# Kernel tuning notes

Measured on AMD Instinct MI355X. Metric: run time of the kernel, lower is better.

## Reference

```python
import jax, jax.numpy as jnp
import numpy as np
from jax import lax

ALPHA = 100.0      # SuperSpike surrogate slope (LIFParameters alpha)
DT = 1e-3          # norse default dt
TAU_SYN_INV = 200.0
TAU_MEM_INV = 100.0
V_TH = 1.0

@jax.custom_vjp
def superspike(x):
    return (x > 0).astype(x.dtype)

def _ss_fwd(x):
    return (x > 0).astype(x.dtype), x

def _ss_bwd(x, g):
    return (g / (ALPHA * jnp.abs(x) + 1.0) ** 2,)

superspike.defvjp(_ss_fwd, _ss_bwd)

def lif_step(inp, v, i):
    # norse lif_step: decay v/i, spike on v_decayed - v_th, reset, then add input current
    v_dec = v + DT * TAU_MEM_INV * (-v + i)
    i_dec = i * (1.0 - DT * TAU_SYN_INV)
    z = superspike(v_dec - V_TH)
    v_new = (1.0 - z) * v_dec  # v_reset = 0
    i_new = i_dec + inp
    return z, v_new, i_new

def li_step(inp, v, i):
    # leaky integrator readout (LILinearCell): returns membrane voltage
    v_new = v + DT * TAU_MEM_INV * (-v + i)
    i_new = i * (1.0 - DT * TAU_SYN_INV) + inp
    return v_new, v_new, i_new

def conv2d(x, w, b):
    y = lax.conv_general_dilated(x, w, (1, 1), 'VALID',
                                 dimension_numbers=('NCHW', 'OIHW', 'NCHW'))
    return y + b[None, :, None, None]

def maxpool2(x):
    return lax.reduce_window(x, -jnp.inf, lax.max, (1, 1, 2, 2), (1, 1, 2, 2), 'VALID')

def setup_inputs() -> dict:
    key = jax.random.key(0)
    ks = jax.random.split(key, 9)
    T, B, C, H = 16, 64, 3, 64
    feats = int(((H - 4) / 2 - 4) / 2)  # 13
    def unif(k, shape, fan_in):
        bound = 1.0 / np.sqrt(fan_in)
        return jax.random.uniform(k, shape, jnp.float32, -bound, bound)
    return {
        'x':  jax.random.normal(ks[0], (T, B, C, H, H), jnp.float32),
        'w1': unif(ks[1], (32, C, 5, 5), C * 25),
        'b1': unif(ks[2], (32,), C * 25),
        'w2': unif(ks[3], (64, 32, 5, 5), 32 * 25),
        'b2': unif(ks[4], (64,), 32 * 25),
        'wf': unif(ks[5], (1024, feats * feats * 64), feats * feats * 64),
        'bf': unif(ks[6], (1024,), feats * feats * 64),
        'wo': unif(ks[7], (10, 1024), 1024),
        'bo': unif(ks[8], (10,), 1024),
    }

def reference(x, w1, b1, w2, b2, wf, bf, wo, bo):
    T, B, C, H, _ = x.shape
    h1 = H - 4           # conv1 out spatial
    p1 = h1 // 2         # pool1
    h2 = p1 - 4          # conv2 out spatial
    p2 = h2 // 2         # pool2 (== features)
    dtype = x.dtype
    zeros = lambda s: jnp.zeros(s, dtype)
    carry0 = (zeros((B, 32, h1, h1)), zeros((B, 32, h1, h1)),   # lif0 v, i
              zeros((B, 64, h2, h2)), zeros((B, 64, h2, h2)),   # lif1 v, i
              zeros((B, 1024)), zeros((B, 1024)),               # lif2 v, i
              zeros((B, 10)), zeros((B, 10)))                   # out  v, i

    def step(carry, xt):
        v0, i0, v1, i1, v2, i2, vo, io = carry
        z = conv2d(xt, w1, b1)
        z, v0, i0 = lif_step(z, v0, i0)
        z = maxpool2(z)
        z = 10.0 * conv2d(z, w2, b2)
        z, v1, i1 = lif_step(z, v1, i1)
        z = maxpool2(z)
        z = z.reshape(B, -1)
        z = z @ wf.T + bf
        z, v2, i2 = lif_step(z, v2, i2)
        inp = jax.nn.relu(z) @ wo.T + bo
        v, vo, io = li_step(inp, vo, io)
        return (v0, i0, v1, i1, v2, i2, vo, io), v

    _, voltages = lax.scan(step, carry0, x)
    return voltages  # [T, B, 10]
```

## Files before the change

kernel.cpp:

```cpp
#include <hip/hip_runtime.h>

typedef __attribute__((ext_vector_type(8))) short short8v;
typedef __attribute__((ext_vector_type(4))) float f32x4;

#define DT_TM 0.1f
#define SYN_DEC 0.8f
#define TT 16
#define BB 64
#define FCK 10816

#define BO_S1   ((size_t)0)
#define BO_S2   ((size_t)29491200)
#define BO_S3   ((size_t)51642368)
#define BO_PART ((size_t)55836672)
#define BO_WH2  BO_PART
#define BO_WL2  (BO_PART + 102400)
#define BO_AFW  (BO_PART + 204800)
#define BO_WHF  ((size_t)72613888)
#define BO_WLF  ((size_t)94765056)
#define BIG_NEED ((size_t)116916224)

#define FO_S1   ((size_t)0)
#define FO_S2   ((size_t)29491200)
#define FO_S3   ((size_t)40566784)
#define FO_PART ((size_t)44761088)
#define FO_V2   ((size_t)51576832)
#define FO_I2   ((size_t)51838976)
#define FO_WH2  FO_PART
#define FO_WL2  (FO_PART + 102400)

__device__ __forceinline__ unsigned short bf16_rne(float f) {
  unsigned int u = __float_as_uint(f);
  return (unsigned short)((u + 0x7FFFu + ((u >> 16) & 1u)) >> 16);
}

__global__ __launch_bounds__(256) void k0_prep(
    const float* __restrict__ w2, unsigned short* __restrict__ whi,
    unsigned short* __restrict__ wlo) {
  int e = blockIdx.x * 256 + threadIdx.x;
  if (e >= 25 * 64 * 32) return;
  int kk = e >> 11;
  int rem = e & 2047;
  int oc = rem >> 5, c = rem & 31;
  float w = w2[(size_t)(oc * 32 + c) * 25 + kk];
  unsigned short hi = bf16_rne(w);
  float fhi = __uint_as_float((unsigned int)hi << 16);
  unsigned short lo = bf16_rne(w - fhi);
  whi[e] = hi;
  wlo[e] = lo;
}

__global__ __launch_bounds__(256) void k0b_wf(
    const float* __restrict__ wf, unsigned short* __restrict__ whiF,
    unsigned short* __restrict__ wloF) {
  size_t e = (size_t)blockIdx.x * 256 + threadIdx.x;
  if (e >= (size_t)1024 * FCK) return;
  float w = wf[e];
  unsigned short hi = bf16_rne(w);
  float fhi = __uint_as_float((unsigned int)hi << 16);
  whiF[e] = hi;
  wloF[e] = bf16_rne(w - fhi);
}

__global__ __launch_bounds__(256) void k0w_prep(
    const float* __restrict__ w1, unsigned short* __restrict__ afw) {
  int e = blockIdx.x * 256 + threadIdx.x;
  if (e >= 9216) return;
  int i = e & 7, l = (e >> 3) & 63, f = e >> 9;
  int sp = f % 3, ks = (f / 3) % 3, mt = f / 9;
  int oc = mt * 16 + (l & 15);
  int tap = (l >> 4) * 8 + i;
  unsigned short out = 0;
  int ky = tap / 6, kx = tap - 6 * ky;
  if (tap < 30 && kx < 5) {
    float v = w1[(oc * 3 + ks) * 25 + ky * 5 + kx];
    unsigned short h = bf16_rne(v);
    if (sp == 0) out = h;
    else {
      float r1 = v - __uint_as_float((unsigned int)h << 16);
      unsigned short m = bf16_rne(r1);
      if (sp == 1) out = m;
      else out = bf16_rne(r1 - __uint_as_float((unsigned int)m << 16));
    }
  }
  afw[e] = out;
}

#define MFMA_BF16 __builtin_amdgcn_mfma_f32_16x16x32_bf16

__global__ __launch_bounds__(256) void k1_mfma(
    const float* __restrict__ x, const unsigned short* __restrict__ afw,
    const float* __restrict__ b1, unsigned char* __restrict__ s1) {
  __shared__ unsigned int Hp[2][18 * 81];
  __shared__ unsigned int Mp[2][18 * 81];
  __shared__ unsigned int Lp[2][18 * 81];
  const int s = blockIdx.x;
  const int b = blockIdx.y;
  const int tid = threadIdx.x;
  const int w = tid >> 6, l = tid & 63;
  const int n = l & 15, tg = l >> 4;
  const int xpix = 16 * w + n;
  const int xcl = (xpix < 60) ? xpix : 59;
  const bool storer = ((n & 1) == 0) && (xpix < 60);

  short8v aw[2][3][3];
#pragma unroll
  for (int mt = 0; mt < 2; ++mt)
#pragma unroll
    for (int ks = 0; ks < 3; ++ks)
#pragma unroll
      for (int sp = 0; sp < 3; ++sp)
        aw[mt][ks][sp] =
            *(const short8v*)(afw + (((mt * 3 + ks) * 3 + sp) * 64 + l) * 8);

  f32x4 bias0 = *(const f32x4*)&b1[tg * 4];
  f32x4 bias1 = *(const f32x4*)&b1[16 + tg * 4];

  int poff[4];
#pragma unroll
  for (int i = 0; i < 4; ++i) {
    int tap = tg * 8 + 2 * i;
    int ky = tap / 6, kx = tap - 6 * ky;
    if (tap >= 30) { ky = 4; kx = 0; }
    poff[i] = ky * 81 + kx;
  }

  const int jrow0 = tid >> 5, jcp0 = tid & 31;
  const int jrow1 = (tid + 256) >> 5;
  const int jrow2 = (tid + 512) >> 5;
  const bool job2 = tid < 64;
  const int slan = (l & 32) | ((l + 1) & 31);

  float vst[2][2][4], ist[2][2][4];
#pragma unroll
  for (int a = 0; a < 2; ++a)
#pragma unroll
    for (int m = 0; m < 2; ++m)
#pragma unroll
      for (int r = 0; r < 4; ++r) { vst[a][m][r] = 0.f; ist[a][m][r] = 0.f; }

  float2 pf0, pf1, pf2;

  auto phaseA = [&](int t) {
    const float* xp = x + ((size_t)(t * BB + b)) * 12288 + (size_t)(2 * s) * 64;
    {
      int c = jrow0 / 6, r = jrow0 - 6 * c;
      pf0 = *(const float2*)(xp + c * 4096 + r * 64 + 2 * jcp0);
    }
    {
      int c = jrow1 / 6, r = jrow1 - 6 * c;
      pf1 = *(const float2*)(xp + c * 4096 + r * 64 + 2 * jcp0);
    }
    if (job2) {
      int c = jrow2 / 6, r = jrow2 - 6 * c;
      pf2 = *(const float2*)(xp + c * 4096 + r * 64 + 2 * jcp0);
    }
  };

  auto phaseB = [&](int bfi) {
    unsigned int* H = Hp[bfi];
    unsigned int* M = Mp[bfi];
    unsigned int* L = Lp[bfi];
#pragma unroll
    for (int j = 0; j < 3; ++j) {
      if (j == 2 && !job2) break;
      float2 v2 = (j == 0) ? pf0 : (j == 1) ? pf1 : pf2;
      int row = (j == 0) ? jrow0 : (j == 1) ? jrow1 : jrow2;
      int cp = jcp0;
      unsigned int h0 = bf16_rne(v2.x);
      float r0 = v2.x - __uint_as_float(h0 << 16);
      unsigned int m0 = bf16_rne(r0);
      unsigned int l0 = bf16_rne(r0 - __uint_as_float(m0 << 16));
      unsigned int h1 = bf16_rne(v2.y);
      float r1 = v2.y - __uint_as_float(h1 << 16);
      unsigned int m1 = bf16_rne(r1);
      unsigned int l1 = bf16_rne(r1 - __uint_as_float(m1 << 16));
      unsigned int hm0 = h0 | (m0 << 16);
      unsigned int hmN = (unsigned int)__shfl((int)hm0, slan);
      unsigned int lN  = (unsigned int)__shfl((int)l0, slan);
      int d = row * 81 + 2 * cp;
      H[d]     = h0 | (h1 << 16);
      H[d + 1] = h1 | (hmN << 16);
      M[d]     = m0 | (m1 << 16);
      M[d + 1] = m1 | (hmN & 0xffff0000u);
      L[d]     = l0 | (l1 << 16);
      L[d + 1] = l1 | (lN << 16);
    }
  };

  phaseA(0);
  phaseB(0);
  __syncthreads();

  for (int t = 0; t < TT; ++t) {
    const int cur = t & 1;
    if (t + 1 < TT) phaseA(t + 1);

    const unsigned int* H = Hp[cur];
    const unsigned int* M = Mp[cur];
    const unsigned int* L = Lp[cur];

    unsigned int pk[2];
#pragma unroll
    for (int nt = 0; nt < 2; ++nt) {
      f32x4 acc0 = (f32x4){0.f, 0.f, 0.f, 0.f};
      f32x4 acc1 = (f32x4){0.f, 0.f, 0.f, 0.f};
#pragma unroll
      for (int ks = 0; ks < 3; ++ks) {
        const int base = (ks * 6 + nt) * 81 + xcl;
        union { unsigned int u[4]; short8v v; } fH, fM, fL;
#pragma unroll
        for (int i = 0; i < 4; ++i) {
          fH.u[i] = H[base + poff[i]];
          fM.u[i] = M[base + poff[i]];
          fL.u[i] = L[base + poff[i]];
        }
        acc0 = MFMA_BF16(aw[0][ks][2], fH.v, acc0, 0, 0, 0);
        acc1 = MFMA_BF16(aw[1][ks][2], fH.v, acc1, 0, 0, 0);
        acc0 = MFMA_BF16(aw[0][ks][1], fM.v, acc0, 0, 0, 0);
        acc1 = MFMA_BF16(aw[1][ks][1], fM.v, acc1, 0, 0, 0);
        acc0 = MFMA_BF16(aw[0][ks][0], fL.v, acc0, 0, 0, 0);
        acc1 = MFMA_BF16(aw[1][ks][0], fL.v, acc1, 0, 0, 0);
        acc0 = MFMA_BF16(aw[0][ks][1], fH.v, acc0, 0, 0, 0);
        acc1 = MFMA_BF16(aw[1][ks][1], fH.v, acc1, 0, 0, 0);
        acc0 = MFMA_BF16(aw[0][ks][0], fM.v, acc0, 0, 0, 0);
        acc1 = MFMA_BF16(aw[1][ks][0], fM.v, acc1, 0, 0, 0);
        acc0 = MFMA_BF16(aw[0][ks][0], fH.v, acc0, 0, 0, 0);
        acc1 = MFMA_BF16(aw[1][ks][0], fH.v, acc1, 0, 0, 0);
      }
      unsigned int nib0 = 0, nib1 = 0;
#pragma unroll
      for (int r = 0; r < 4; ++r) {
        float inp = acc0[r] + bias0[r];
        float vd = vst[nt][0][r] + DT_TM * (ist[nt][0][r] - vst[nt][0][r]);
        float id = SYN_DEC * ist[nt][0][r];
        bool z = vd > 1.0f;
        vst[nt][0][r] = z ? 0.f : vd;
        ist[nt][0][r] = id + inp;
        nib0 |= (z ? 1u : 0u) << r;

        float inp1 = acc1[r] + bias1[r];
        float vd1 = vst[nt][1][r] + DT_TM * (ist[nt][1][r] - vst[nt][1][r]);
        float id1 = SYN_DEC * ist[nt][1][r];
        bool z1 = vd1 > 1.0f;
        vst[nt][1][r] = z1 ? 0.f : vd1;
        ist[nt][1][r] = id1 + inp1;
        nib1 |= (z1 ? 1u : 0u) << r;
      }
      pk[nt] = nib0 | (nib1 << 4);
    }
    unsigned int pr = pk[0] | pk[1];
    unsigned int pc = pr | __shfl_xor(pr, 1);
    if (storer) {
      size_t base =
          (((size_t)(t * BB + b)) * 900 + (size_t)s * 30 + (xpix >> 1)) * 32 +
          tg * 4;
      unsigned int lo = pc & 0xFu, hi = (pc >> 4) & 0xFu;
      *(unsigned int*)&s1[base] =
          (lo & 1u) | ((lo & 2u) << 7) | ((lo & 4u) << 14) | ((lo & 8u) << 21);
      *(unsigned int*)&s1[base + 16] =
          (hi & 1u) | ((hi & 2u) << 7) | ((hi & 4u) << 14) | ((hi & 8u) << 21);
    }
    if (t + 1 < TT) {
      phaseB((t + 1) & 1);
      __syncthreads();
    }
  }
}

__global__ __launch_bounds__(256) void k1_conv1(
    const float* __restrict__ x, const float* __restrict__ w1,
    const float* __restrict__ b1, unsigned char* __restrict__ s1) {
  __shared__ float xs[3 * 64 * 68];
  const int oc = blockIdx.x;
  const int b  = blockIdx.y;
  const int tid = threadIdx.x;
  const bool valid = tid < 225;
  const int py0 = (tid / 15) * 2;
  const int px0 = (tid % 15) * 2;
  const int br = 2 * py0;
  const int bc = 2 * px0;

  float v[16], cur[16];
#pragma unroll
  for (int j = 0; j < 16; ++j) { v[j] = 0.f; cur[j] = 0.f; }
  const float bias = b1[oc];

  for (int t = 0; t < TT; ++t) {
    const float* xp = x + ((size_t)(t * BB + b)) * 12288;
#pragma unroll
    for (int k = 0; k < 12; ++k) {
      int e = tid + k * 256;
      int row = e >> 4, c4 = e & 15;
      ((float4*)xs)[row * 17 + c4] = ((const float4*)xp)[e];
    }
    __syncthreads();

    if (valid) {
      float acc[4][4];
#pragma unroll
      for (int r = 0; r < 4; ++r)
#pragma unroll
        for (int s = 0; s < 4; ++s) acc[r][s] = 0.f;

#pragma unroll
      for (int c = 0; c < 3; ++c) {
        const float* wp = w1 + (oc * 3 + c) * 25;
        float wv[25];
#pragma unroll
        for (int j = 0; j < 25; ++j) wv[j] = wp[j];
#pragma unroll
        for (int ri = 0; ri < 8; ++ri) {
          const float* rowp = &xs[(c * 64 + br + ri) * 68 + bc];
          float4 ra = *(const float4*)rowp;
          float4 rb = *(const float4*)(rowp + 4);
          float row[8] = {ra.x, ra.y, ra.z, ra.w, rb.x, rb.y, rb.z, rb.w};
#pragma unroll
          for (int r = 0; r < 4; ++r) {
            int ky = ri - r;
            if (ky >= 0 && ky < 5) {
#pragma unroll
              for (int kx = 0; kx < 5; ++kx) {
                float w = wv[ky * 5 + kx];
#pragma unroll
                for (int s = 0; s < 4; ++s) acc[r][s] += w * row[s + kx];
              }
            }
          }
        }
      }

      unsigned char pz00 = 0, pz01 = 0, pz10 = 0, pz11 = 0;
#pragma unroll
      for (int r = 0; r < 4; ++r)
#pragma unroll
        for (int s = 0; s < 4; ++s) {
          int j = r * 4 + s;
          float vd = v[j] + DT_TM * (cur[j] - v[j]);
          float id = SYN_DEC * cur[j];
          float inp = acc[r][s] + bias;
          bool z = vd > 1.0f;
          v[j] = z ? 0.f : vd;
          cur[j] = id + inp;
          if (z) {
            if (r < 2) { if (s < 2) pz00 = 1; else pz01 = 1; }
            else       { if (s < 2) pz10 = 1; else pz11 = 1; }
          }
        }
      size_t pixb = ((size_t)(t * BB + b)) * 900;
      s1[(pixb + (size_t)py0 * 30 + px0) * 32 + oc]           = pz00;
      s1[(pixb + (size_t)py0 * 30 + px0 + 1) * 32 + oc]       = pz01;
      s1[(pixb + (size_t)(py0 + 1) * 30 + px0) * 32 + oc]     = pz10;
      s1[(pixb + (size_t)(py0 + 1) * 30 + px0 + 1) * 32 + oc] = pz11;
    }
    __syncthreads();
  }
}

__device__ __forceinline__ void k2_stage_load(
    const unsigned char* __restrict__ s1, unsigned int (&pf)[6],
    int t, int b, int y0, int inRows) {
  const int tid = threadIdx.x;
  const unsigned char* sp =
      s1 + (((size_t)(t * BB + b)) * 900 + (size_t)y0 * 30) * 32;
  const int nelem = inRows * 240;
#pragma unroll
  for (int i = 0; i < 6; ++i) {
    int e = tid + i * 512;
    if (e < nelem) pf[i] = *(const unsigned int*)(sp + (size_t)e * 4);
  }
}

__device__ __forceinline__ void k2_stage_write(
    unsigned short* sl, const unsigned int (&pf)[6], int inRows) {
  const int tid = threadIdx.x;
  const int nelem = inRows * 240;
#pragma unroll
  for (int i = 0; i < 6; ++i) {
    int e = tid + i * 512;
    if (e < nelem) {
      unsigned int w = pf[i];
      unsigned int lo = ((w & 0xFFu) ? 0x3F80u : 0u) |
                        ((w & 0xFF00u) ? 0x3F800000u : 0u);
      unsigned int hi = ((w & 0xFF0000u) ? 0x3F80u : 0u) |
                        ((w & 0xFF000000u) ? 0x3F800000u : 0u);
      ((unsigned int*)sl)[e * 2]     = lo;
      ((unsigned int*)sl)[e * 2 + 1] = hi;
    }
  }
}

template<typename ST>
__device__ __forceinline__ void k2_pool(
    ST* __restrict__ s2, const unsigned char* zbuf, int t, int b, int y0, int R) {
  const int tid = threadIdx.x;
  const int prr = R >> 1;
  const int pcount = prr * 13 * 64;
  ST* s2p = s2 + ((size_t)(t * BB + b)) * 64 * 169;
  const int gpy0 = y0 >> 1;
  const ST one = (ST)((sizeof(ST) == 2) ? 0x3F80 : 1);
  for (int e = tid; e < pcount; e += 512) {
    int oc = e & 63, pp = e >> 6;
    int ppy = pp / 13, ppx = pp - ppy * 13;
    int base = (2 * ppy * 26 + 2 * ppx) * 68 + oc;
    unsigned char z = (unsigned char)(zbuf[base] | zbuf[base + 68] |
                      zbuf[base + 26 * 68] | zbuf[base + 26 * 68 + 68]);
    s2p[(size_t)oc * 169 + (gpy0 + ppy) * 13 + ppx] = z ? one : (ST)0;
  }
}

template<int NT>
__device__ __forceinline__ void k2_wave(
    const unsigned short* sl, float* Vst, float* Ist, unsigned char* zbuf,
    const unsigned short* __restrict__ whi, const unsigned short* __restrict__ wlo,
    const float* __restrict__ b2, int og, int mi, int q, int n,
    int ntstart, int npos) {
  int baddr[NT], pcl[NT];
  f32x4 acc[NT];
#pragma unroll
  for (int j = 0; j < NT; ++j) {
    int pl = (ntstart + j) * 16 + n;
    if (pl > npos - 1) pl = npos - 1;
    pcl[j] = pl;
    int ry = pl / 26, xx = pl - ry * 26;
    baddr[j] = (ry * 30 + xx) * 32 + q * 8;
    acc[j] = (f32x4){0.f, 0.f, 0.f, 0.f};
  }
  const int abase = (og * 32 + n) * 32 + q * 8 + mi * 512;
#pragma unroll 5
  for (int kk = 0; kk < 25; ++kk) {
    const int ky = kk / 5, kx = kk - (kk / 5) * 5;
    const int off = (ky * 30 + kx) * 32;
    short8v ah = *(const short8v*)(whi + kk * 2048 + abase);
    short8v al = *(const short8v*)(wlo + kk * 2048 + abase);
#pragma unroll
    for (int j = 0; j < NT; ++j) {
      short8v bv = *(const short8v*)(sl + baddr[j] + off);
      acc[j] = MFMA_BF16(al, bv, acc[j], 0, 0, 0);
      acc[j] = MFMA_BF16(ah, bv, acc[j], 0, 0, 0);
    }
  }
  const f32x4 bia = *(const f32x4*)&b2[og * 32 + mi * 16 + q * 4];
#pragma unroll
  for (int j = 0; j < NT; ++j) {
    int p = pcl[j];
    int sidx = p * 68 + og * 32 + mi * 16 + q * 4;
    f32x4 v4 = *(f32x4*)&Vst[sidx];
    f32x4 i4 = *(f32x4*)&Ist[sidx];
    f32x4 a = acc[j];
    unsigned char zr[4];
#pragma unroll
    for (int r = 0; r < 4; ++r) {
      float vd = v4[r] + DT_TM * (i4[r] - v4[r]);
      float id = SYN_DEC * i4[r];
      float inp = 10.f * (a[r] + bia[r]);
      bool z = vd > 1.0f;
      v4[r] = z ? 0.f : vd;
      i4[r] = id + inp;
      zr[r] = z ? 1 : 0;
    }
    *(f32x4*)&Vst[sidx] = v4;
    *(f32x4*)&Ist[sidx] = i4;
    *(uchar4*)&zbuf[sidx] = make_uchar4(zr[0], zr[1], zr[2], zr[3]);
  }
}

template<typename ST>
__global__ __launch_bounds__(512) void k2_mfma_l(
    const unsigned char* __restrict__ s1, const unsigned short* __restrict__ whi,
    const unsigned short* __restrict__ wlo, const float* __restrict__ b2,
    ST* __restrict__ s2) {
  __shared__ unsigned short sl[12 * 30 * 32];
  __shared__ float Vst[208 * 68];
  __shared__ float Ist[208 * 68];
  __shared__ unsigned char zbuf[208 * 68];
  const int quad = blockIdx.x, b = blockIdx.y;
  const int tid = threadIdx.x;
  const int wid = tid >> 6, l = tid & 63;
  const int og = wid & 1, mi = (wid >> 1) & 1, nc = wid >> 2;
  const int q = l >> 4, n = l & 15;
  const int y0 = (quad == 0) ? 0 : (2 + quad * 6);
  const int R  = (quad == 0) ? 8 : 6;
  const int inRows = R + 4;
  const int npos = R * 26;

  for (int e = tid; e < 208 * 68; e += 512) { Vst[e] = 0.f; Ist[e] = 0.f; }

  unsigned int pf[6];
  k2_stage_load(s1, pf, 0, b, y0, inRows);
  k2_stage_write(sl, pf, inRows);
  __syncthreads();

  for (int t = 0; t < TT; ++t) {
    if (t + 1 < TT) k2_stage_load(s1, pf, t + 1, b, y0, inRows);

    if (quad == 0) {
      if (nc == 0)
        k2_wave<7>(sl, Vst, Ist, zbuf, whi, wlo, b2, og, mi, q, n, 0, npos);
      else
        k2_wave<6>(sl, Vst, Ist, zbuf, whi, wlo, b2, og, mi, q, n, 7, npos);
    } else {
      k2_wave<5>(sl, Vst, Ist, zbuf, whi, wlo, b2, og, mi, q, n, nc * 5, npos);
    }
    __syncthreads();

    k2_pool<ST>(s2, zbuf, t, b, y0, R);
    if (t + 1 < TT) k2_stage_write(sl, pf, inRows);
    __syncthreads();
  }
}

__global__ __launch_bounds__(512) void k3g_fc(
    const unsigned short* __restrict__ s2,
    const unsigned short* __restrict__ whiF,
    const unsigned short* __restrict__ wloF,
    float* __restrict__ part) {
  __shared__ __align__(16) unsigned short As[128][72];
  __shared__ __align__(16) unsigned short Bh[128][72];
  __shared__ __align__(16) unsigned short Bl[128][72];
  const int tid = threadIdx.x;
  const int w = tid >> 6, l = tid & 63;
  const int mh = w & 1, nq = w >> 1;
  const int lr = l & 15, lk = l >> 4;
  const int n0 = blockIdx.x * 128, m0 = blockIdx.y * 128;
  const int ks = blockIdx.z;
  const int s_begin = (169 * ks) >> 2, s_end = (169 * (ks + 1)) >> 2;

  const int arow = tid >> 2, aseg = tid & 3;
  const unsigned short* ap = s2 + (size_t)(m0 + arow) * FCK + aseg * 16;
  unsigned short* aq = &As[0][0] + arow * 72 + aseg * 16;
  const int barr = tid >> 8, brem = tid & 255;
  const int bn = brem >> 1, bhalf = brem & 1;
  const unsigned short* bp =
      (barr ? wloF : whiF) + (size_t)(n0 + bn) * FCK + bhalf * 32;
  unsigned short* bq = (barr ? &Bl[0][0] : &Bh[0][0]) + bn * 72 + bhalf * 32;

  f32x4 acc[4][2];
#pragma unroll
  for (int mt = 0; mt < 4; ++mt)
#pragma unroll
    for (int nt = 0; nt < 2; ++nt) acc[mt][nt] = (f32x4){0.f, 0.f, 0.f, 0.f};

  for (int s = s_begin; s < s_end; ++s) {
    const size_t k0 = (size_t)s * 64;
    short8v a0 = *(const short8v*)(ap + k0);
    short8v a1 = *(const short8v*)(ap + k0 + 8);
    short8v b0 = *(const short8v*)(bp + k0);
    short8v b1 = *(const short8v*)(bp + k0 + 8);
    short8v b2v = *(const short8v*)(bp + k0 + 16);
    short8v b3 = *(const short8v*)(bp + k0 + 24);
    __syncthreads();
    *(short8v*)(aq)      = a0;
    *(short8v*)(aq + 8)  = a1;
    *(short8v*)(bq)      = b0;
    *(short8v*)(bq + 8)  = b1;
    *(short8v*)(bq + 16) = b2v;
    *(short8v*)(bq + 24) = b3;
    __syncthreads();
#pragma unroll
    for (int kt = 0; kt < 2; ++kt) {
      short8v bh0 = *(const short8v*)&Bh[nq * 32 + lr][kt * 32 + lk * 8];
      short8v bh1 = *(const short8v*)&Bh[nq * 32 + 16 + lr][kt * 32 + lk * 8];
      short8v bl0 = *(const short8v*)&Bl[nq * 32 + lr][kt * 32 + lk * 8];
      short8v bl1 = *(const short8v*)&Bl[nq * 32 + 16 + lr][kt * 32 + lk * 8];
#pragma unroll
      for (int mt = 0; mt < 4; ++mt) {
        short8v af = *(const short8v*)&As[mh * 64 + mt * 16 + lr][kt * 32 + lk * 8];
        acc[mt][0] = MFMA_BF16(af, bh0, acc[mt][0], 0, 0, 0);
        acc[mt][0] = MFMA_BF16(af, bl0, acc[mt][0], 0, 0, 0);
        acc[mt][1] = MFMA_BF16(af, bh1, acc[mt][1], 0, 0, 0);
        acc[mt][1] = MFMA_BF16(af, bl1, acc[mt][1], 0, 0, 0);
      }
    }
  }
  float* pp = part + ((size_t)ks << 20);
#pragma unroll
  for (int mt = 0; mt < 4; ++mt)
#pragma unroll
    for (int nt = 0; nt < 2; ++nt) {
      int mrow = m0 + mh * 64 + mt * 16 + lk * 4;
      int ncol = n0 + nq * 32 + nt * 16 + lr;
#pragma unroll
      for (int r = 0; r < 4; ++r)
        pp[(size_t)(mrow + r) * 1024 + ncol] = acc[mt][nt][r];
    }
}

__global__ __launch_bounds__(256) void k3r_lif2(
    const float* __restrict__ part, const float* __restrict__ bf,
    float* __restrict__ s3) {
  int e = blockIdx.x * 256 + threadIdx.x;
  int n = e & 1023;
  const float bias = bf[n];
  float v = 0.f, cur = 0.f;
  for (int t = 0; t < TT; ++t) {
    size_t idx = ((size_t)(t * BB) << 10) + e;
    float g = part[idx] + part[idx + (1u << 20)] +
              part[idx + (2u << 20)] + part[idx + (3u << 20)] + bias;
    float vd = v + DT_TM * (cur - v);
    float id = SYN_DEC * cur;
    bool sp = vd > 1.0f;
    v = sp ? 0.f : vd;
    cur = id + g;
    s3[(size_t)t * 65536 + e] = sp ? 1.f : 0.f;
  }
}

__global__ __launch_bounds__(256) void k3a_fc(
    const unsigned char* __restrict__ s2, const float* __restrict__ wf,
    float* __restrict__ part, int t) {
  __shared__ float As[16][68];
  __shared__ float Bs[16][68];
  const int nt = blockIdx.x;
  const int ks = blockIdx.y;
  const int tid = threadIdx.x;
  const int N0 = nt * 64;
  const int kbase = ks * 416;
  const unsigned char* A = s2 + (size_t)t * BB * FCK;

  const int lm = tid >> 2;
  const int kq = tid & 3;
  const int m0 = (tid >> 4) << 2;
  const int n0 = (tid & 15) << 2;

  float acc[4][4];
#pragma unroll
  for (int i = 0; i < 4; ++i)
#pragma unroll
    for (int j = 0; j < 4; ++j) acc[i][j] = 0.f;

  for (int step = 0; step < 26; ++step) {
    int k0 = kbase + step * 16;
    uchar4 a4 = *(const uchar4*)&A[(size_t)lm * FCK + k0 + kq * 4];
    float4 b4 = *(const float4*)&wf[(size_t)(N0 + lm) * FCK + k0 + kq * 4];
    __syncthreads();
    As[kq * 4 + 0][lm] = (float)a4.x;
    As[kq * 4 + 1][lm] = (float)a4.y;
    As[kq * 4 + 2][lm] = (float)a4.z;
    As[kq * 4 + 3][lm] = (float)a4.w;
    Bs[kq * 4 + 0][lm] = b4.x;
    Bs[kq * 4 + 1][lm] = b4.y;
    Bs[kq * 4 + 2][lm] = b4.z;
    Bs[kq * 4 + 3][lm] = b4.w;
    __syncthreads();
#pragma unroll
    for (int kk = 0; kk < 16; ++kk) {
      float4 av = *(const float4*)&As[kk][m0];
      float4 bv = *(const float4*)&Bs[kk][n0];
      float a0 = av.x, a1 = av.y, a2 = av.z, a3 = av.w;
      acc[0][0] += a0 * bv.x; acc[0][1] += a0 * bv.y; acc[0][2] += a0 * bv.z; acc[0][3] += a0 * bv.w;
      acc[1][0] += a1 * bv.x; acc[1][1] += a1 * bv.y; acc[1][2] += a1 * bv.z; acc[1][3] += a1 * bv.w;
      acc[2][0] += a2 * bv.x; acc[2][1] += a2 * bv.y; acc[2][2] += a2 * bv.z; acc[2][3] += a2 * bv.w;
      acc[3][0] += a3 * bv.x; acc[3][1] += a3 * bv.y; acc[3][2] += a3 * bv.z; acc[3][3] += a3 * bv.w;
    }
  }
#pragma unroll
  for (int i = 0; i < 4; ++i)
#pragma unroll
    for (int j = 0; j < 4; ++j)
      part[((size_t)(ks * 64 + m0 + i)) * 1024 + N0 + n0 + j] = acc[i][j];
}

__global__ __launch_bounds__(256) void k3b_lif2(
    const float* __restrict__ part, const float* __restrict__ bf,
    float* __restrict__ v2, float* __restrict__ i2,
    float* __restrict__ s3, int t) {
  int e = blockIdx.x * 256 + threadIdx.x;
  int n = e & 1023;
  float s = 0.f;
#pragma unroll
  for (int ks = 0; ks < 26; ++ks) s += part[(size_t)ks * 65536 + e];
  float z = s + bf[n];
  float vv = v2[e], ii = i2[e];
  float vd = vv + DT_TM * (ii - vv);
  float id = SYN_DEC * ii;
  bool sp = vd > 1.0f;
  v2[e] = sp ? 0.f : vd;
  i2[e] = id + z;
  s3[(size_t)t * 65536 + e] = sp ? 1.f : 0.f;
}

__global__ __launch_bounds__(320) void k4_out(
    const float* __restrict__ s3, const float* __restrict__ wo,
    const float* __restrict__ bo, float* __restrict__ out) {
  const int b = blockIdx.x;
  const int g = threadIdx.x >> 5;
  const int l = threadIdx.x & 31;
  float vv = 0.f, ii = 0.f;
  const float bg = bo[g];
  for (int t = 0; t < TT; ++t) {
    const float* zp = s3 + ((size_t)t * BB + b) * 1024;
    const float* wp = wo + g * 1024;
    float p = 0.f;
#pragma unroll 8
    for (int j = l; j < 1024; j += 32) p += zp[j] * wp[j];
#pragma unroll
    for (int off = 16; off; off >>= 1) p += __shfl_down(p, off, 32);
    float inp = p + bg;
    float vn = vv + DT_TM * (ii - vv);
    if (l == 0) out[(size_t)(t * BB + b) * 10 + g] = vn;
    ii = SYN_DEC * ii + inp;
    vv = vn;
  }
}

extern "C" void kernel_launch(void* const* d_in, const int* in_sizes, int n_in,
                              void* d_out, int out_size, void* d_ws, size_t ws_size,
                              hipStream_t stream) {
  (void)in_sizes; (void)n_in; (void)out_size;
  const float* x  = (const float*)d_in[0];
  const float* w1 = (const float*)d_in[1];
  const float* b1 = (const float*)d_in[2];
  const float* w2 = (const float*)d_in[3];
  const float* b2 = (const float*)d_in[4];
  const float* wf = (const float*)d_in[5];
  const float* bf = (const float*)d_in[6];
  const float* wo = (const float*)d_in[7];
  const float* bo = (const float*)d_in[8];
  float* out = (float*)d_out;
  char* ws = (char*)d_ws;

  if (ws_size >= BIG_NEED) {
    unsigned char*  s1   = (unsigned char*)(ws + BO_S1);
    unsigned short* s2   = (unsigned short*)(ws + BO_S2);
    float*          s3   = (float*)(ws + BO_S3);
    float*          part = (float*)(ws + BO_PART);
    unsigned short* wh2  = (unsigned short*)(ws + BO_WH2);
    unsigned short* wl2  = (unsigned short*)(ws + BO_WL2);
    unsigned short* afw  = (unsigned short*)(ws + BO_AFW);
    unsigned short* whiF = (unsigned short*)(ws + BO_WHF);
    unsigned short* wloF = (unsigned short*)(ws + BO_WLF);

    k0_prep<<<dim3(200), 256, 0, stream>>>(w2, wh2, wl2);
    k0w_prep<<<dim3(36), 256, 0, stream>>>(w1, afw);
    k0b_wf<<<dim3(43264), 256, 0, stream>>>(wf, whiF, wloF);
    k1_mfma<<<dim3(30, 64), 256, 0, stream>>>(x, afw, b1, s1);
    k2_mfma_l<unsigned short><<<dim3(4, 64), 512, 0, stream>>>(
        s1, wh2, wl2, b2, s2);
    k3g_fc<<<dim3(8, 8, 4), 512, 0, stream>>>(s2, whiF, wloF, part);
    k3r_lif2<<<dim3(256), 256, 0, stream>>>(part, bf, s3);
    k4_out<<<dim3(64), 320, 0, stream>>>(s3, wo, bo, out);
  } else {
    unsigned char*  s1   = (unsigned char*)(ws + FO_S1);
    unsigned char*  s2   = (unsigned char*)(ws + FO_S2);
    float*          s3   = (float*)(ws + FO_S3);
    float*          part = (float*)(ws + FO_PART);
    float*          v2   = (float*)(ws + FO_V2);
    float*          i2   = (float*)(ws + FO_I2);
    unsigned short* wh2  = (unsigned short*)(ws + FO_WH2);
    unsigned short* wl2  = (unsigned short*)(ws + FO_WL2);

    hipMemsetAsync(v2, 0, 2 * 65536 * sizeof(float), stream);
    k0_prep<<<dim3(200), 256, 0, stream>>>(w2, wh2, wl2);
    k1_conv1<<<dim3(32, 64), 256, 0, stream>>>(x, w1, b1, s1);
    k2_mfma_l<unsigned char><<<dim3(4, 64), 512, 0, stream>>>(s1, wh2, wl2, b2, s2);
    for (int t = 0; t < TT; ++t) {
      k3a_fc<<<dim3(16, 26), 256, 0, stream>>>(s2, wf, part, t);
      k3b_lif2<<<dim3(256), 256, 0, stream>>>(part, bf, v2, i2, s3, t);
    }
    k4_out<<<dim3(64), 320, 0, stream>>>(s3, wo, bo, out);
  }
}
```

Before: 444.2 us.

## Split conv1 MFMA output-channel tiles across two waves per pixel group

Doubles the conv1 block from 256 to 512 threads so that each wave handles one 16-channel half of the output instead of both. Per-wave MFMA chain length, weight registers and LIF state are halved, and the input staging work is spread over more threads. The cost is that each channel half reloads the same LDS B-fragments, LDS reads per block roughly double, and the larger block may limit occupancy.

Result: slower. 514.4 us (+15.8%).

```diff
diff --git a/kernel.cpp b/kernel.cpp
--- a/kernel.cpp
+++ b/kernel.cpp
@@ -88,7 +88,7 @@
 
 #define MFMA_BF16 __builtin_amdgcn_mfma_f32_16x16x32_bf16
 
-__global__ __launch_bounds__(256) void k1_mfma(
+__global__ __launch_bounds__(512) void k1_mfma(
     const float* __restrict__ x, const unsigned short* __restrict__ afw,
     const float* __restrict__ b1, unsigned char* __restrict__ s1) {
   __shared__ unsigned int Hp[2][18 * 81];
@@ -97,24 +97,22 @@
   const int s = blockIdx.x;
   const int b = blockIdx.y;
   const int tid = threadIdx.x;
-  const int w = tid >> 6, l = tid & 63;
+  const int wid = tid >> 6, l = tid & 63;
+  const int mt = wid & 1, w = wid >> 1;
   const int n = l & 15, tg = l >> 4;
   const int xpix = 16 * w + n;
   const int xcl = (xpix < 60) ? xpix : 59;
   const bool storer = ((n & 1) == 0) && (xpix < 60);
 
-  short8v aw[2][3][3];
-#pragma unroll
-  for (int mt = 0; mt < 2; ++mt)
-#pragma unroll
-    for (int ks = 0; ks < 3; ++ks)
-#pragma unroll
-      for (int sp = 0; sp < 3; ++sp)
-        aw[mt][ks][sp] =
-            *(const short8v*)(afw + (((mt * 3 + ks) * 3 + sp) * 64 + l) * 8);
-
-  f32x4 bias0 = *(const f32x4*)&b1[tg * 4];
-  f32x4 bias1 = *(const f32x4*)&b1[16 + tg * 4];
+  short8v aw[3][3];
+#pragma unroll
+  for (int ks = 0; ks < 3; ++ks)
+#pragma unroll
+    for (int sp = 0; sp < 3; ++sp)
+      aw[ks][sp] =
+          *(const short8v*)(afw + (((mt * 3 + ks) * 3 + sp) * 64 + l) * 8);
+
+  f32x4 bias = *(const f32x4*)&b1[mt * 16 + tg * 4];
 
   int poff[4];
 #pragma unroll
@@ -126,20 +124,17 @@
   }
 
   const int jrow0 = tid >> 5, jcp0 = tid & 31;
-  const int jrow1 = (tid + 256) >> 5;
-  const int jrow2 = (tid + 512) >> 5;
-  const bool job2 = tid < 64;
+  const int jrow1 = (tid + 512) >> 5;
+  const bool job1 = tid < 64;
   const int slan = (l & 32) | ((l + 1) & 31);
 
-  float vst[2][2][4], ist[2][2][4];
+  float vst[2][4], ist[2][4];
 #pragma unroll
   for (int a = 0; a < 2; ++a)
 #pragma unroll
-    for (int m = 0; m < 2; ++m)
-#pragma unroll
-      for (int r = 0; r < 4; ++r) { vst[a][m][r] = 0.f; ist[a][m][r] = 0.f; }
-
-  float2 pf0, pf1, pf2;
+    for (int r = 0; r < 4; ++r) { vst[a][r] = 0.f; ist[a][r] = 0.f; }
+
+  float2 pf0, pf1;
 
   auto phaseA = [&](int t) {
     const float* xp = x + ((size_t)(t * BB + b)) * 12288 + (size_t)(2 * s) * 64;
@@ -147,13 +142,9 @@
       int c = jrow0 / 6, r = jrow0 - 6 * c;
       pf0 = *(const float2*)(xp + c * 4096 + r * 64 + 2 * jcp0);
     }
-    {
+    if (job1) {
       int c = jrow1 / 6, r = jrow1 - 6 * c;
       pf1 = *(const float2*)(xp + c * 4096 + r * 64 + 2 * jcp0);
-    }
-    if (job2) {
-      int c = jrow2 / 6, r = jrow2 - 6 * c;
-      pf2 = *(const float2*)(xp + c * 4096 + r * 64 + 2 * jcp0);
     }
   };
 
@@ -162,10 +153,10 @@
     unsigned int* M = Mp[bfi];
     unsigned int* L = Lp[bfi];
 #pragma unroll
-    for (int j = 0; j < 3; ++j) {
-      if (j == 2 && !job2) break;
-      float2 v2 = (j == 0) ? pf0 : (j == 1) ? pf1 : pf2;
-      int row = (j == 0) ? jrow0 : (j == 1) ? jrow1 : jrow2;
+    for (int j = 0; j < 2; ++j) {
+      if (j == 1 && !job1) break;
+      float2 v2 = (j == 0) ? pf0 : pf1;
+      int row = (j == 0) ? jrow0 : jrow1;
       int cp = jcp0;
       unsigned int h0 = bf16_rne(v2.x);
       float r0 = v2.x - __uint_as_float(h0 << 16);
@@ -203,8 +194,7 @@
     unsigned int pk[2];
 #pragma unroll
     for (int nt = 0; nt < 2; ++nt) {
-      f32x4 acc0 = (f32x4){0.f, 0.f, 0.f, 0.f};
-      f32x4 acc1 = (f32x4){0.f, 0.f, 0.f, 0.f};
+      f32x4 acc = (f32x4){0.f, 0.f, 0.f, 0.f};
 #pragma unroll
       for (int ks = 0; ks < 3; ++ks) {
         const int base = (ks * 6 + nt) * 81 + xcl;
@@ -215,51 +205,34 @@
           fM.u[i] = M[base + poff[i]];
           fL.u[i] = L[base + poff[i]];
         }
-        acc0 = MFMA_BF16(aw[0][ks][2], fH.v, acc0, 0, 0, 0);
-        acc1 = MFMA_BF16(aw[1][ks][2], fH.v, acc1, 0, 0, 0);
-        acc0 = MFMA_BF16(aw[0][ks][1], fM.v, acc0, 0, 0, 0);
-        acc1 = MFMA_BF16(aw[1][ks][1], fM.v, acc1, 0, 0, 0);
-        acc0 = MFMA_BF16(aw[0][ks][0], fL.v, acc0, 0, 0, 0);
-        acc1 = MFMA_BF16(aw[1][ks][0], fL.v, acc1, 0, 0, 0);
-        acc0 = MFMA_BF16(aw[0][ks][1], fH.v, acc0, 0, 0, 0);
-        acc1 = MFMA_BF16(aw[1][ks][1], fH.v, acc1, 0, 0, 0);
-        acc0 = MFMA_BF16(aw[0][ks][0], fM.v, acc0, 0, 0, 0);
-        acc1 = MFMA_BF16(aw[1][ks][0], fM.v, acc1, 0, 0, 0);
-        acc0 = MFMA_BF16(aw[0][ks][0], fH.v, acc0, 0, 0, 0);
-        acc1 = MFMA_BF16(aw[1][ks][0], fH.v, acc1, 0, 0, 0);
+        acc = MFMA_BF16(aw[ks][2], fH.v, acc, 0, 0, 0);
+        acc = MFMA_BF16(aw[ks][1], fM.v, acc, 0, 0, 0);
+        acc = MFMA_BF16(aw[ks][0], fL.v, acc, 0, 0, 0);
+        acc = MFMA_BF16(aw[ks][1], fH.v, acc, 0, 0, 0);
+        acc = MFMA_BF16(aw[ks][0], fM.v, acc, 0, 0, 0);
+        acc = MFMA_BF16(aw[ks][0], fH.v, acc, 0, 0, 0);
       }
-      unsigned int nib0 = 0, nib1 = 0;
+      unsigned int nib = 0;
 #pragma unroll
       for (int r = 0; r < 4; ++r) {
-        float inp = acc0[r] + bias0[r];
-        float vd = vst[nt][0][r] + DT_TM * (ist[nt][0][r] - vst[nt][0][r]);
-        float id = SYN_DEC * ist[nt][0][r];
+        float inp = acc[r] + bias[r];
+        float vd = vst[nt][r] + DT_TM * (ist[nt][r] - vst[nt][r]);
+        float id = SYN_DEC * ist[nt][r];
         bool z = vd > 1.0f;
-        vst[nt][0][r] = z ? 0.f : vd;
-        ist[nt][0][r] = id + inp;
-        nib0 |= (z ? 1u : 0u) << r;
-
-        float inp1 = acc1[r] + bias1[r];
-        float vd1 = vst[nt][1][r] + DT_TM * (ist[nt][1][r] - vst[nt][1][r]);
-        float id1 = SYN_DEC * ist[nt][1][r];
-        bool z1 = vd1 > 1.0f;
-        vst[nt][1][r] = z1 ? 0.f : vd1;
-        ist[nt][1][r] = id1 + inp1;
-        nib1 |= (z1 ? 1u : 0u) << r;
+        vst[nt][r] = z ? 0.f : vd;
+        ist[nt][r] = id + inp;
+        nib |= (z ? 1u : 0u) << r;
       }
-      pk[nt] = nib0 | (nib1 << 4);
+      pk[nt] = nib;
     }
     unsigned int pr = pk[0] | pk[1];
     unsigned int pc = pr | __shfl_xor(pr, 1);
     if (storer) {
       size_t base =
           (((size_t)(t * BB + b)) * 900 + (size_t)s * 30 + (xpix >> 1)) * 32 +
-          tg * 4;
-      unsigned int lo = pc & 0xFu, hi = (pc >> 4) & 0xFu;
+          mt * 16 + tg * 4;
       *(unsigned int*)&s1[base] =
-          (lo & 1u) | ((lo & 2u) << 7) | ((lo & 4u) << 14) | ((lo & 8u) << 21);
-      *(unsigned int*)&s1[base + 16] =
-          (hi & 1u) | ((hi & 2u) << 7) | ((hi & 4u) << 14) | ((hi & 8u) << 21);
+          (pc & 1u) | ((pc & 2u) << 7) | ((pc & 4u) << 14) | ((pc & 8u) << 21);
     }
     if (t + 1 < TT) {
       phaseB((t + 1) & 1);
@@ -734,7 +707,7 @@
     k0_prep<<<dim3(200), 256, 0, stream>>>(w2, wh2, wl2);
     k0w_prep<<<dim3(36), 256, 0, stream>>>(w1, afw);
     k0b_wf<<<dim3(43264), 256, 0, stream>>>(wf, whiF, wloF);
-    k1_mfma<<<dim3(30, 64), 256, 0, stream>>>(x, afw, b1, s1);
+    k1_mfma<<<dim3(30, 64), 512, 0, stream>>>(x, afw, b1, s1);
     k2_mfma_l<unsigned short><<<dim3(4, 64), 512, 0, stream>>>(
         s1, wh2, wl2, b2, s2);
     k3g_fc<<<dim3(8, 8, 4), 512, 0, stream>>>(s2, whiF, wloF, part);
```
